# Performance work log

Hardware: AMD Instinct MI355X
Metric: run time of the kernel (lower is better)

## Reference

```python
import jax, jax.numpy as jnp
import numpy as np

W, L, D = 4096, 32, 256
WORD_VOCAB, CHR_VOCAB = 50000, 128


def conv1d(x, w, b):
    # x: [N, C_in, T], w: [C_out, C_in, 3], padding=1 (same)
    y = jax.lax.conv_general_dilated(
        x, w, window_strides=(1,), padding=[(1, 1)],
        dimension_numbers=("NCW", "OIW", "NCW"))
    return y + b[None, :, None]


def setup_inputs() -> dict:
    key = jax.random.key(0)
    ks = jax.random.split(key, 12)
    words = jax.random.randint(ks[0], (W,), 0, WORD_VOCAB, dtype=jnp.int32)
    words_in_char = jax.random.randint(ks[1], (W, L), 0, CHR_VOCAB, dtype=jnp.int32)
    s = 0.02
    word_emb = (jax.random.normal(ks[2], (WORD_VOCAB, D), jnp.float32) * s).at[0].set(0.0)  # padding_idx=0
    chr_emb = (jax.random.normal(ks[3], (CHR_VOCAB, D), jnp.float32) * s).at[0].set(0.0)
    conv_chr_w = jax.random.normal(ks[4], (D, D, 3), jnp.float32) * s
    conv_chr_b = jax.random.normal(ks[5], (D,), jnp.float32) * s
    conv_sent_w = jax.random.normal(ks[6], (2 * D, 2 * D, 3), jnp.float32) * s
    conv_sent_b = jax.random.normal(ks[7], (2 * D,), jnp.float32) * s
    w1 = jax.random.normal(ks[8], (4 * D, 2 * D), jnp.float32) * s
    b1 = jax.random.normal(ks[9], (4 * D,), jnp.float32) * s
    w2 = jax.random.normal(ks[10], (2, 4 * D), jnp.float32) * s
    b2 = jax.random.normal(ks[11], (2,), jnp.float32) * s
    return dict(words=words, words_in_char=words_in_char,
                word_emb=word_emb, chr_emb=chr_emb,
                conv_chr_w=conv_chr_w, conv_chr_b=conv_chr_b,
                conv_sent_w=conv_sent_w, conv_sent_b=conv_sent_b,
                w1=w1, b1=b1, w2=w2, b2=b2)


def reference(words, words_in_char, word_emb, chr_emb,
              conv_chr_w, conv_chr_b, conv_sent_w, conv_sent_b,
              w1, b1, w2, b2):
    # word embeddings: [W, D]
    vector_wrds = word_emb[words]
    # char path, batched over all words (equivalent to the per-word loop):
    ch = chr_emb[words_in_char]                      # [W, L, D]
    ch = jnp.transpose(ch, (0, 2, 1))                # [W, D, L]
    wc = conv1d(ch, conv_chr_w, conv_chr_b)          # [W, D, L]
    vector_wchs = jnp.max(wc, axis=2)                # [W, D]
    # sentence conv over the word axis
    u = jnp.concatenate([vector_wrds, vector_wchs], axis=1)  # [W, 2D]
    u = u.T[None, :, :]                              # [1, 2D, W]
    r = conv1d(u, conv_sent_w, conv_sent_b)          # [1, 2D, W]
    r = jnp.max(r, axis=2)                           # [1, 2D]
    h = jnp.tanh(r @ w1.T + b1)                      # [1, 4D]
    return h @ w2.T + b2                             # [1, 2]
```

## Files before the change

### kernel.cpp

```cpp
#include <hip/hip_runtime.h>
#include <hip/hip_bf16.h>
#include <math.h>

#define NW 4096
#define NL 32
#define ND 256
#define ND2 512

typedef __attribute__((ext_vector_type(8))) short short8;
typedef __attribute__((ext_vector_type(4))) short short4v;
typedef __attribute__((ext_vector_type(4))) float floatx4;

__device__ inline float bfval(short s) {
  union { unsigned u; float f; } v;
  v.u = ((unsigned)(unsigned short)s) << 16;
  return v.f;
}
__device__ inline short bf16s(float x) {
  __hip_bfloat16 h = __float2bfloat16(x);
  return *reinterpret_cast<short*>(&h);
}


__global__ __launch_bounds__(256) void prep_kernel(
    const float* __restrict__ conv_sent_w, const float* __restrict__ conv_chr_w,
    float* __restrict__ wT, short* __restrict__ Wb,
    short* __restrict__ u_base) {
  int b = blockIdx.x;
  int tid = threadIdx.x;
  if (b < 1024) {
    int g = b * 256 + tid;
    int co = g >> 9, ci = g & 511;
    const float* s = conv_sent_w + co * 1536 + ci * 3;
    float f0 = s[0], f1 = s[1], f2 = s[2];
    int o = co * 512 + ci;
    Wb[o] = bf16s(f0);
    Wb[262144 + o] = bf16s(f1);
    Wb[524288 + o] = bf16s(f2);
  } else if (b < 1280) {
    int g = (b - 1024) * 256 + tid;
    int ci = g >> 8, co = g & 255;
    const float* s = conv_chr_w + co * 768 + ci * 3;
    float f0 = s[0], f1 = s[1], f2 = s[2];
    int o = ci * 256 + co;
    wT[o] = f0;
    wT[65536 + o] = f1;
    wT[131072 + o] = f2;
  } else {
    u_base[tid] = 0;
    u_base[tid + 256] = 0;
    u_base[4097 * 512 + tid] = 0;
    u_base[4097 * 512 + tid + 256] = 0;
  }
}

__global__ __launch_bounds__(256) void table_kernel(
    const float* __restrict__ chr_emb, const float* __restrict__ wT,
    __hip_bfloat16* __restrict__ Tb) {
  __shared__ float s_e[4][256];
  int k = blockIdx.x >> 5;
  int c0 = (blockIdx.x & 31) * 4;
  int co = threadIdx.x;
#pragma unroll
  for (int j = 0; j < 4; ++j) s_e[j][co] = chr_emb[(c0 + j) * 256 + co];
  __syncthreads();
  const float* wk = wT + k * 65536;
  float a0 = 0.f, a1 = 0.f, a2 = 0.f, a3 = 0.f;
#pragma unroll 8
  for (int ci = 0; ci < 256; ++ci) {
    float w = wk[ci * 256 + co];
    a0 = fmaf(s_e[0][ci], w, a0);
    a1 = fmaf(s_e[1][ci], w, a1);
    a2 = fmaf(s_e[2][ci], w, a2);
    a3 = fmaf(s_e[3][ci], w, a3);
  }
  int base = ((co >> 6) * 3 + k) * 8192 + (co & 63);
  Tb[base + (c0 + 0) * 64] = __float2bfloat16(a0);
  Tb[base + (c0 + 1) * 64] = __float2bfloat16(a1);
  Tb[base + (c0 + 2) * 64] = __float2bfloat16(a2);
  Tb[base + (c0 + 3) * 64] = __float2bfloat16(a3);
}

__global__ __launch_bounds__(256) void char_word_kernel(
    const int* __restrict__ words, const int* __restrict__ wic,
    const __hip_bfloat16* __restrict__ Tb, const float* __restrict__ word_emb,
    const float* __restrict__ bias, short* __restrict__ u0s) {
  __shared__ short sT[3 * 128 * 64];
  __shared__ int s_wic[64 * 32];
  __shared__ int s_wid[64];
  int ct = blockIdx.x >> 6;
  int w0 = (blockIdx.x & 63) * 64;
  int tid = threadIdx.x;
  {
    const uint4* src = (const uint4*)((const short*)Tb + ct * 24576);
    uint4* dst = (uint4*)sT;
#pragma unroll
    for (int i = 0; i < 12; ++i) dst[tid + i * 256] = src[tid + i * 256];
    const int4* wsrc = (const int4*)(wic + w0 * 32);
    int4* wdst = (int4*)s_wic;
    wdst[tid] = wsrc[tid];
    wdst[tid + 256] = wsrc[tid + 256];
    if (tid < 64) s_wid[tid] = words[w0 + tid];
  }
  __syncthreads();
  const int co4 = (tid & 15) * 4;
  const int slot = tid >> 4;
  const short* T0 = sT;
  const short* T1 = sT + 8192;
  const short* T2 = sT + 16384;
  const float4 bb = *(const float4*)(bias + ct * 64 + co4);
  for (int wi = 0; wi < 4; ++wi) {
    int wl = slot * 4 + wi;
    {
      float4 we = *(const float4*)(word_emb + s_wid[wl] * ND + ct * 64 + co4);
      short4v ws;
      ws.x = bf16s(we.x); ws.y = bf16s(we.y); ws.z = bf16s(we.z); ws.w = bf16s(we.w);
      *(short4v*)&u0s[(w0 + wl) * ND2 + ct * 64 + co4] = ws;
    }
    int cc[32];
    {
      const int4* cp = (const int4*)(s_wic + wl * 32);
#pragma unroll
      for (int i = 0; i < 8; ++i) {
        int4 v = cp[i];
        cc[i * 4] = v.x; cc[i * 4 + 1] = v.y; cc[i * 4 + 2] = v.z; cc[i * 4 + 3] = v.w;
      }
    }
    float m0 = -INFINITY, m1 = -INFINITY, m2 = -INFINITY, m3 = -INFINITY;
#pragma unroll
    for (int t = 0; t < NL; ++t) {
      short4v q1 = *(const short4v*)&T1[cc[t] * 64 + co4];
      float s0 = bfval(q1.x), s1 = bfval(q1.y), s2 = bfval(q1.z), s3 = bfval(q1.w);
      if (t > 0) {
        short4v q0 = *(const short4v*)&T0[cc[t - 1] * 64 + co4];
        s0 += bfval(q0.x); s1 += bfval(q0.y); s2 += bfval(q0.z); s3 += bfval(q0.w);
      }
      if (t < NL - 1) {
        short4v q2 = *(const short4v*)&T2[cc[t + 1] * 64 + co4];
        s0 += bfval(q2.x); s1 += bfval(q2.y); s2 += bfval(q2.z); s3 += bfval(q2.w);
      }
      m0 = fmaxf(m0, s0); m1 = fmaxf(m1, s1);
      m2 = fmaxf(m2, s2); m3 = fmaxf(m3, s3);
    }
    short4v res;
    res.x = bf16s(m0 + bb.x); res.y = bf16s(m1 + bb.y);
    res.z = bf16s(m2 + bb.z); res.w = bf16s(m3 + bb.w);
    *(short4v*)&u0s[(w0 + wl) * ND2 + ND + ct * 64 + co4] = res;
  }
}

__global__ __launch_bounds__(256, 2) void sent_conv_mfma(
    const __hip_bfloat16* __restrict__ u0,
    const __hip_bfloat16* __restrict__ Wb,
    float* __restrict__ partial) {
  __shared__ short As[64 * 64];
  __shared__ short Bs[64 * 64];
  __shared__ float sm[4][32];
  const int tid = threadIdx.x;
  const int t0 = blockIdx.x * 64;
  const int co0 = blockIdx.y * 64;
  const int wave = tid >> 6, lane = tid & 63;
  const int wy = wave >> 1, wx = wave & 1;
  const int m = lane & 15, q = lane >> 4;

  floatx4 acc[2][2];
#pragma unroll
  for (int i = 0; i < 2; ++i)
#pragma unroll
    for (int j = 0; j < 2; ++j) acc[i][j] = (floatx4){0.f, 0.f, 0.f, 0.f};

  int aoff[2][2], boff[2][2];
#pragma unroll
  for (int kk = 0; kk < 2; ++kk) {
#pragma unroll
    for (int i = 0; i < 2; ++i) {
      int row = wy * 32 + i * 16 + m;
      aoff[kk][i] = row * 64 + (((kk * 4 + q) ^ (row & 7)) * 8);
      row = wx * 32 + i * 16 + m;
      boff[kk][i] = row * 64 + (((kk * 4 + q) ^ (row & 7)) * 8);
    }
  }

  const int sc = tid & 7, sr = tid >> 3;
  const int swc = (sc ^ (sr & 7)) * 8;
  const short* WbS = (const short*)Wb;
  const short* uS = (const short*)u0;

  for (int s = 0; s < 24; ++s) {
    int k = s >> 3, ci0 = (s & 7) << 6;
    const short* WbK = WbS + k * 262144 + (co0 + sr) * 512 + ci0 + sc * 8;
    const short* uK = uS + (t0 + sr + k - 1) * 512 + ci0 + sc * 8;
    uint4 a0 = *(const uint4*)(WbK);
    uint4 a1 = *(const uint4*)(WbK + 32 * 512);
    uint4 b0 = *(const uint4*)(uK);
    uint4 b1 = *(const uint4*)(uK + 32 * 512);
    *(uint4*)&As[sr * 64 + swc] = a0;
    *(uint4*)&As[(sr + 32) * 64 + swc] = a1;
    *(uint4*)&Bs[sr * 64 + swc] = b0;
    *(uint4*)&Bs[(sr + 32) * 64 + swc] = b1;
    __syncthreads();
#pragma unroll
    for (int kk = 0; kk < 2; ++kk) {
      short8 av0 = *(const short8*)&As[aoff[kk][0]];
      short8 av1 = *(const short8*)&As[aoff[kk][1]];
      short8 bv0 = *(const short8*)&Bs[boff[kk][0]];
      short8 bv1 = *(const short8*)&Bs[boff[kk][1]];
      acc[0][0] = __builtin_amdgcn_mfma_f32_16x16x32_bf16(av0, bv0, acc[0][0], 0, 0, 0);
      acc[0][1] = __builtin_amdgcn_mfma_f32_16x16x32_bf16(av0, bv1, acc[0][1], 0, 0, 0);
      acc[1][0] = __builtin_amdgcn_mfma_f32_16x16x32_bf16(av1, bv0, acc[1][0], 0, 0, 0);
      acc[1][1] = __builtin_amdgcn_mfma_f32_16x16x32_bf16(av1, bv1, acc[1][1], 0, 0, 0);
    }
    __syncthreads();
  }

#pragma unroll
  for (int i = 0; i < 2; ++i)
#pragma unroll
    for (int r = 0; r < 4; ++r) {
      float x = fmaxf(acc[i][0][r], acc[i][1][r]);
#pragma unroll
      for (int off = 1; off < 16; off <<= 1)
        x = fmaxf(x, __shfl_xor(x, off, 64));
      if (m == 0) sm[wave][i * 16 + q * 4 + r] = x;
    }
  __syncthreads();
  if (tid < 64) {
    int whalf = tid >> 5;
    float v = fmaxf(sm[whalf * 2 + 0][tid & 31], sm[whalf * 2 + 1][tid & 31]);
    partial[(co0 + tid) * 64 + blockIdx.x] = v;
  }
}

__global__ __launch_bounds__(512) void fc1_kernel(
    const float* __restrict__ partial, const float* __restrict__ bs,
    const float* __restrict__ w1, const float* __restrict__ b1,
    float* __restrict__ h) {
  __shared__ float s_r[512];
  int tid = threadIdx.x;
  {
    const float4* p = (const float4*)(partial + tid * 64);
    float mm = -INFINITY;
#pragma unroll
    for (int j = 0; j < 16; ++j) {
      float4 v = p[j];
      mm = fmaxf(mm, fmaxf(fmaxf(v.x, v.y), fmaxf(v.z, v.w)));
    }
    s_r[tid] = mm + bs[tid];
  }
  __syncthreads();
  int wave = tid >> 6, lane = tid & 63;
  int o = blockIdx.x * 8 + wave;
  const float4* wv = (const float4*)(w1 + o * 512 + lane * 8);
  const float4* rv = (const float4*)(s_r + lane * 8);
  float4 w0 = wv[0], w1v = wv[1];
  float4 r0 = rv[0], r1 = rv[1];
  float acc = w0.x * r0.x + w0.y * r0.y + w0.z * r0.z + w0.w * r0.w +
              w1v.x * r1.x + w1v.y * r1.y + w1v.z * r1.z + w1v.w * r1.w;
#pragma unroll
  for (int off = 32; off >= 1; off >>= 1) acc += __shfl_down(acc, off, 64);
  if (lane == 0) h[o] = tanhf(acc + b1[o]);
}

__global__ __launch_bounds__(128) void fc2_kernel(
    const float* __restrict__ h, const float* __restrict__ w2,
    const float* __restrict__ b2, float* __restrict__ out) {
  int tid = threadIdx.x;
  int o = tid >> 6;
  int lane = tid & 63;
  float acc = 0.f;
#pragma unroll
  for (int j = 0; j < 16; ++j)
    acc = fmaf(w2[o * 1024 + lane + j * 64], h[lane + j * 64], acc);
#pragma unroll
  for (int off = 32; off >= 1; off >>= 1) acc += __shfl_down(acc, off, 64);
  if (lane == 0) out[o] = acc + b2[o];
}

extern "C" void kernel_launch(void* const* d_in, const int* in_sizes, int n_in,
                              void* d_out, int out_size, void* d_ws, size_t ws_size,
                              hipStream_t stream) {
  const int*   words       = (const int*)d_in[0];
  const int*   wic         = (const int*)d_in[1];
  const float* word_emb    = (const float*)d_in[2];
  const float* chr_emb     = (const float*)d_in[3];
  const float* conv_chr_w  = (const float*)d_in[4];
  const float* conv_chr_b  = (const float*)d_in[5];
  const float* conv_sent_w = (const float*)d_in[6];
  const float* conv_sent_b = (const float*)d_in[7];
  const float* w1          = (const float*)d_in[8];
  const float* b1          = (const float*)d_in[9];
  const float* w2          = (const float*)d_in[10];
  const float* b2          = (const float*)d_in[11];
  float* out = (float*)d_out;

  float* ws    = (float*)d_ws;
  float* wT    = ws;
  float* part  = wT + 196608;
  float* h_buf = part + 32768;
  short* Tb    = (short*)(h_buf + 1024);
  short* u_base = Tb + 98304;
  short* u0s   = u_base + 512;
  __hip_bfloat16* u0 = (__hip_bfloat16*)u0s;
  short* Wb    = u_base + 4098 * 512;

  prep_kernel<<<1281, 256, 0, stream>>>(conv_sent_w, conv_chr_w, wT, Wb, u_base);
  table_kernel<<<96, 256, 0, stream>>>(chr_emb, wT, (__hip_bfloat16*)Tb);
  char_word_kernel<<<256, 256, 0, stream>>>(words, wic, (const __hip_bfloat16*)Tb,
                                            word_emb, conv_chr_b, u0s);
  sent_conv_mfma<<<dim3(64, 8), 256, 0, stream>>>(u0, (const __hip_bfloat16*)Wb, part);
  fc1_kernel<<<128, 512, 0, stream>>>(part, conv_sent_b, w1, b1, h_buf);
  fc2_kernel<<<1, 128, 0, stream>>>(h_buf, w2, b2, out);
}
```

Measured before the change: 161.1 us.

## Restructure sentence conv to single-wave blocks with shared halo tile and fuse fc kernels

The sentence conv kernel now runs one wave per 64x64 output tile. It loads a 66-row input halo into shared memory once per channel half and reuses it for all three conv taps. Weight fragments are read straight from global into registers with a one-step prefetch instead of being staged through LDS. fc1 and fc2 are merged into one kernel, where the last block, found through an atomic counter reset in prep, computes the final output. This drops a launch and most LDS staging and barriers, but leaves only one wave per block, which risks lower latency hiding and higher register pressure.

Measured after the change: 197.8 us. 22.8% more time.

```diff
diff --git a/kernel.cpp b/kernel.cpp
--- a/kernel.cpp
+++ b/kernel.cpp
@@ -25,7 +25,7 @@
 __global__ __launch_bounds__(256) void prep_kernel(
     const float* __restrict__ conv_sent_w, const float* __restrict__ conv_chr_w,
     float* __restrict__ wT, short* __restrict__ Wb,
-    short* __restrict__ u_base) {
+    short* __restrict__ u_base, int* __restrict__ counter) {
   int b = blockIdx.x;
   int tid = threadIdx.x;
   if (b < 1024) {
@@ -51,6 +51,7 @@
     u_base[tid + 256] = 0;
     u_base[4097 * 512 + tid] = 0;
     u_base[4097 * 512 + tid + 256] = 0;
+    if (tid == 0) counter[0] = 0;
   }
 }
 
@@ -149,93 +150,94 @@
   }
 }
 
-__global__ __launch_bounds__(256, 2) void sent_conv_mfma(
+__global__ __launch_bounds__(64) void sent_conv_mfma(
     const __hip_bfloat16* __restrict__ u0,
     const __hip_bfloat16* __restrict__ Wb,
     float* __restrict__ partial) {
-  __shared__ short As[64 * 64];
-  __shared__ short Bs[64 * 64];
-  __shared__ float sm[4][32];
-  const int tid = threadIdx.x;
+  __shared__ short Bs[66 * 256];
+  const int lane = threadIdx.x;
   const int t0 = blockIdx.x * 64;
   const int co0 = blockIdx.y * 64;
-  const int wave = tid >> 6, lane = tid & 63;
-  const int wy = wave >> 1, wx = wave & 1;
   const int m = lane & 15, q = lane >> 4;
 
-  floatx4 acc[2][2];
-#pragma unroll
-  for (int i = 0; i < 2; ++i)
-#pragma unroll
-    for (int j = 0; j < 2; ++j) acc[i][j] = (floatx4){0.f, 0.f, 0.f, 0.f};
-
-  int aoff[2][2], boff[2][2];
-#pragma unroll
-  for (int kk = 0; kk < 2; ++kk) {
-#pragma unroll
-    for (int i = 0; i < 2; ++i) {
-      int row = wy * 32 + i * 16 + m;
-      aoff[kk][i] = row * 64 + (((kk * 4 + q) ^ (row & 7)) * 8);
-      row = wx * 32 + i * 16 + m;
-      boff[kk][i] = row * 64 + (((kk * 4 + q) ^ (row & 7)) * 8);
-    }
-  }
-
-  const int sc = tid & 7, sr = tid >> 3;
-  const int swc = (sc ^ (sr & 7)) * 8;
+  floatx4 acc[4][4];
+#pragma unroll
+  for (int i = 0; i < 4; ++i)
+#pragma unroll
+    for (int j = 0; j < 4; ++j) acc[i][j] = (floatx4){0.f, 0.f, 0.f, 0.f};
+
+  const short* uS = (const short*)u0;
   const short* WbS = (const short*)Wb;
-  const short* uS = (const short*)u0;
-
-  for (int s = 0; s < 24; ++s) {
-    int k = s >> 3, ci0 = (s & 7) << 6;
-    const short* WbK = WbS + k * 262144 + (co0 + sr) * 512 + ci0 + sc * 8;
-    const short* uK = uS + (t0 + sr + k - 1) * 512 + ci0 + sc * 8;
-    uint4 a0 = *(const uint4*)(WbK);
-    uint4 a1 = *(const uint4*)(WbK + 32 * 512);
-    uint4 b0 = *(const uint4*)(uK);
-    uint4 b1 = *(const uint4*)(uK + 32 * 512);
-    *(uint4*)&As[sr * 64 + swc] = a0;
-    *(uint4*)&As[(sr + 32) * 64 + swc] = a1;
-    *(uint4*)&Bs[sr * 64 + swc] = b0;
-    *(uint4*)&Bs[(sr + 32) * 64 + swc] = b1;
-    __syncthreads();
-#pragma unroll
-    for (int kk = 0; kk < 2; ++kk) {
-      short8 av0 = *(const short8*)&As[aoff[kk][0]];
-      short8 av1 = *(const short8*)&As[aoff[kk][1]];
-      short8 bv0 = *(const short8*)&Bs[boff[kk][0]];
-      short8 bv1 = *(const short8*)&Bs[boff[kk][1]];
-      acc[0][0] = __builtin_amdgcn_mfma_f32_16x16x32_bf16(av0, bv0, acc[0][0], 0, 0, 0);
-      acc[0][1] = __builtin_amdgcn_mfma_f32_16x16x32_bf16(av0, bv1, acc[0][1], 0, 0, 0);
-      acc[1][0] = __builtin_amdgcn_mfma_f32_16x16x32_bf16(av1, bv0, acc[1][0], 0, 0, 0);
-      acc[1][1] = __builtin_amdgcn_mfma_f32_16x16x32_bf16(av1, bv1, acc[1][1], 0, 0, 0);
-    }
-    __syncthreads();
-  }
-
-#pragma unroll
-  for (int i = 0; i < 2; ++i)
+  const int sc = lane & 31, sr0 = lane >> 5;
+
+  short8 af[4], afn[4];
+  {
+    const short* base = WbS + (co0 + m) * 512 + q * 8;
+#pragma unroll
+    for (int i = 0; i < 4; ++i) af[i] = *(const short8*)(base + i * 16 * 512);
+  }
+
+  for (int it = 0; it < 48; ++it) {
+    int half = it / 24;
+    int r = it - half * 24;
+    int k = r >> 3;
+    int cil = (r & 7) * 32;
+    if (r == 0) {
+      __syncthreads();
+      const short* src = uS + (t0 - 1) * 512 + half * 256 + sc * 8;
+#pragma unroll
+      for (int rr = sr0; rr < 66; rr += 2) {
+        uint4 v = *(const uint4*)(src + rr * 512);
+        *(uint4*)&Bs[rr * 256 + ((sc ^ (rr & 7)) * 8)] = v;
+      }
+      __syncthreads();
+    }
+    if (it + 1 < 48) {
+      int itn = it + 1;
+      int hn = itn / 24;
+      int rn = itn - hn * 24;
+      const short* base = WbS + (rn >> 3) * 262144 + (co0 + m) * 512 +
+                          hn * 256 + (rn & 7) * 32 + q * 8;
+#pragma unroll
+      for (int i = 0; i < 4; ++i) afn[i] = *(const short8*)(base + i * 16 * 512);
+    }
+    short8 bf[4];
+#pragma unroll
+    for (int j = 0; j < 4; ++j) {
+      int row = j * 16 + m + k;
+      int ch = ((cil >> 3) + q) ^ (row & 7);
+      bf[j] = *(const short8*)&Bs[row * 256 + ch * 8];
+    }
+#pragma unroll
+    for (int i = 0; i < 4; ++i)
+#pragma unroll
+      for (int j = 0; j < 4; ++j)
+        acc[i][j] = __builtin_amdgcn_mfma_f32_16x16x32_bf16(af[i], bf[j], acc[i][j], 0, 0, 0);
+#pragma unroll
+    for (int i = 0; i < 4; ++i) af[i] = afn[i];
+  }
+
+#pragma unroll
+  for (int i = 0; i < 4; ++i)
 #pragma unroll
     for (int r = 0; r < 4; ++r) {
-      float x = fmaxf(acc[i][0][r], acc[i][1][r]);
+      float x = fmaxf(fmaxf(acc[i][0][r], acc[i][1][r]),
+                      fmaxf(acc[i][2][r], acc[i][3][r]));
 #pragma unroll
       for (int off = 1; off < 16; off <<= 1)
         x = fmaxf(x, __shfl_xor(x, off, 64));
-      if (m == 0) sm[wave][i * 16 + q * 4 + r] = x;
-    }
-  __syncthreads();
-  if (tid < 64) {
-    int whalf = tid >> 5;
-    float v = fmaxf(sm[whalf * 2 + 0][tid & 31], sm[whalf * 2 + 1][tid & 31]);
-    partial[(co0 + tid) * 64 + blockIdx.x] = v;
-  }
-}
-
-__global__ __launch_bounds__(512) void fc1_kernel(
+      if (m == 0) partial[(co0 + i * 16 + q * 4 + r) * 64 + blockIdx.x] = x;
+    }
+}
+
+__global__ __launch_bounds__(512) void fc_kernel(
     const float* __restrict__ partial, const float* __restrict__ bs,
     const float* __restrict__ w1, const float* __restrict__ b1,
-    float* __restrict__ h) {
+    const float* __restrict__ w2, const float* __restrict__ b2,
+    float* __restrict__ h, int* __restrict__ counter,
+    float* __restrict__ out) {
   __shared__ float s_r[512];
+  __shared__ int s_last;
   int tid = threadIdx.x;
   {
     const float4* p = (const float4*)(partial + tid * 64);
@@ -258,22 +260,27 @@
               w1v.x * r1.x + w1v.y * r1.y + w1v.z * r1.z + w1v.w * r1.w;
 #pragma unroll
   for (int off = 32; off >= 1; off >>= 1) acc += __shfl_down(acc, off, 64);
-  if (lane == 0) h[o] = tanhf(acc + b1[o]);
-}
-
-__global__ __launch_bounds__(128) void fc2_kernel(
-    const float* __restrict__ h, const float* __restrict__ w2,
-    const float* __restrict__ b2, float* __restrict__ out) {
-  int tid = threadIdx.x;
-  int o = tid >> 6;
-  int lane = tid & 63;
-  float acc = 0.f;
-#pragma unroll
-  for (int j = 0; j < 16; ++j)
-    acc = fmaf(w2[o * 1024 + lane + j * 64], h[lane + j * 64], acc);
-#pragma unroll
-  for (int off = 32; off >= 1; off >>= 1) acc += __shfl_down(acc, off, 64);
-  if (lane == 0) out[o] = acc + b2[o];
+  if (lane == 0) {
+    h[o] = tanhf(acc + b1[o]);
+    __threadfence();
+  }
+  __syncthreads();
+  if (tid == 0) s_last = (atomicAdd(counter, 1) == 127) ? 1 : 0;
+  __syncthreads();
+  if (s_last) {
+    __threadfence();
+    if (tid < 128) {
+      int o2 = tid >> 6;
+      int l = tid & 63;
+      float a2 = 0.f;
+#pragma unroll
+      for (int j = 0; j < 16; ++j)
+        a2 = fmaf(w2[o2 * 1024 + l + j * 64], h[l + j * 64], a2);
+#pragma unroll
+      for (int off = 32; off >= 1; off >>= 1) a2 += __shfl_down(a2, off, 64);
+      if (l == 0) out[o2] = a2 + b2[o2];
+    }
+  }
 }
 
 extern "C" void kernel_launch(void* const* d_in, const int* in_sizes, int n_in,
@@ -297,17 +304,19 @@
   float* wT    = ws;
   float* part  = wT + 196608;
   float* h_buf = part + 32768;
-  short* Tb    = (short*)(h_buf + 1024);
+  int*   cnt   = (int*)(h_buf + 1024);
+  short* Tb    = (short*)(cnt + 256);
   short* u_base = Tb + 98304;
   short* u0s   = u_base + 512;
   __hip_bfloat16* u0 = (__hip_bfloat16*)u0s;
   short* Wb    = u_base + 4098 * 512;
 
-  prep_kernel<<<1281, 256, 0, stream>>>(conv_sent_w, conv_chr_w, wT, Wb, u_base);
+  prep_kernel<<<1281, 256, 0, stream>>>(conv_sent_w, conv_chr_w, wT, Wb,
+                                        u_base, cnt);
   table_kernel<<<96, 256, 0, stream>>>(chr_emb, wT, (__hip_bfloat16*)Tb);
   char_word_kernel<<<256, 256, 0, stream>>>(words, wic, (const __hip_bfloat16*)Tb,
                                             word_emb, conv_chr_b, u0s);
-  sent_conv_mfma<<<dim3(64, 8), 256, 0, stream>>>(u0, (const __hip_bfloat16*)Wb, part);
-  fc1_kernel<<<128, 512, 0, stream>>>(part, conv_sent_b, w1, b1, h_buf);
-  fc2_kernel<<<1, 128, 0, stream>>>(h_buf, w2, b2, out);
-}
+  sent_conv_mfma<<<dim3(64, 8), 64, 0, stream>>>(u0, (const __hip_bfloat16*)Wb, part);
+  fc_kernel<<<128, 512, 0, stream>>>(part, conv_sent_b, w1, b1, w2, b2,
+                                     h_buf, cnt, out);
+}
```
